# Performance work log

Measured on AMD Instinct MI355X. Metric: run time of the kernel, lower is better.

The kernel has to match this reference:

```python
import jax, jax.numpy as jnp
import numpy as np

N = 100000      # nodes (words + docs)
E = 1600000     # edges
D_IN = 256      # input feature dim
H = 64          # hidden dim
C = 20          # num classes
NDOC = 10000    # doc nodes


def setup_inputs() -> dict:
    key = jax.random.key(0)
    ks = jax.random.split(key, 16)
    inp = {
        "x": jax.random.normal(ks[0], (N, D_IN), dtype=jnp.float32),
        "edge_weight": jax.random.uniform(ks[1], (E,), dtype=jnp.float32),
        "W1": jax.random.normal(ks[2], (D_IN, H), dtype=jnp.float32) * (1.0 / np.sqrt(D_IN)),
        "b1": jnp.zeros((H,), jnp.float32),
        "W2": jax.random.normal(ks[3], (H, H), dtype=jnp.float32) * (1.0 / np.sqrt(H)),
        "b2": jnp.zeros((H,), jnp.float32),
        "W3": jax.random.normal(ks[4], (H, H), dtype=jnp.float32) * (1.0 / np.sqrt(H)),
        "b3": jnp.zeros((H,), jnp.float32),
        "Wp": jax.random.normal(ks[5], (H, H), dtype=jnp.float32) * (1.0 / np.sqrt(H)),
        "bp": jnp.zeros((H,), jnp.float32),
        "Wc": jax.random.normal(ks[6], (H, C), dtype=jnp.float32) * (1.0 / np.sqrt(H)),
        "bc": jnp.zeros((C,), jnp.float32),
        "edge_index": jax.random.randint(ks[7], (2, E), 0, N, dtype=jnp.int32),
        "doc_idx": jnp.sort(jax.random.randint(ks[8], (NDOC,), 0, N, dtype=jnp.int32)),
    }
    return inp


def reference(x, edge_weight, W1, b1, W2, b2, W3, b3, Wp, bp, Wc, bc, edge_index, doc_idx):
    n = x.shape[0]
    src, dst = edge_index[0], edge_index[1]
    loop = jnp.arange(n, dtype=src.dtype)
    rows = jnp.concatenate([src, loop])          # sources (incl. self-loops)
    cols = jnp.concatenate([dst, loop])          # targets
    w = jnp.concatenate([edge_weight, jnp.ones((n,), x.dtype)])
    # symmetric GCN normalization: D^-1/2 (A + I) D^-1/2
    deg = jax.ops.segment_sum(w, cols, num_segments=n)
    deg_safe = jnp.where(deg > 0, deg, 1.0)
    dinv = jnp.where(deg > 0, jax.lax.rsqrt(deg_safe), 0.0)
    norm = dinv[rows] * w * dinv[cols]           # [E+N]

    def conv(h, W, b):
        h = h @ W                                # transform first (PyG GCNConv)
        msg = h[rows] * norm[:, None]            # gather + weight  [E+N, H]
        return jax.ops.segment_sum(msg, cols, num_segments=n) + b

    h = jax.nn.relu(conv(x, W1, b1))             # dropout = identity (eval mode)
    h = jax.nn.relu(conv(h, W2, b2))
    h = jax.nn.relu(conv(h, W3, b3))
    d = h[doc_idx]                               # [NDOC, H]
    d = jax.nn.relu(d @ Wp + bp)
    return d @ Wc + bc                           # [NDOC, C]
```

## Files before the change

kernel.cpp:

```cpp
#include <hip/hip_runtime.h>

#define H 64
#define PAD 48
#define WFIX 262144.0f
#define WFIX_INV (1.0f / 262144.0f)


__global__ __launch_bounds__(256) void k_init(unsigned int* packed, int n) {
    int i = blockIdx.x * 256 + threadIdx.x;
    if (i < n) packed[i] = 0u;
}


__global__ __launch_bounds__(256) void k_fused(const int* __restrict__ src,
                                               const int* __restrict__ dst,
                                               const float* __restrict__ ew,
                                               unsigned int* packed,
                                               int2* __restrict__ csr,
                                               int e_total,
                                               const float* __restrict__ A,
                                               const float* __restrict__ B,
                                               float* __restrict__ out, int M) {
    __shared__ float As[64][68];
    __shared__ float Bs[64][64];
    int tid = threadIdx.x;

    int ebase = blockIdx.x * 1024 + tid;
#pragma unroll
    for (int j = 0; j < 4; ++j) {
        int e = ebase + j * 256;
        if (e < e_total) {
            int d = dst[e];
            float w = ew[e];
            unsigned int enc = (1u << 24) | (unsigned int)(w * WFIX + 0.5f);
            unsigned int old = atomicAdd(&packed[d], enc);
            unsigned int r = old >> 24;
            if (r < PAD) csr[(size_t)d * PAD + r] = make_int2(src[e], __float_as_int(w));
        }
    }

    const int K = 256;
    int brow = blockIdx.x * 64;
    int ct = tid & 15, rt = tid >> 4;
    int c4 = ct * 4, r4 = rt * 4;
    int lrow = tid >> 4;
    int lk4 = (tid & 15) * 4;
    float acc[4][4] = {{0.f}};

    for (int k0 = 0; k0 < K; k0 += 64) {
#pragma unroll
        for (int rr = 0; rr < 64; rr += 16) {
            int row = brow + rr + lrow;
            float4 va = make_float4(0.f, 0.f, 0.f, 0.f);
            if (row < M) va = *(const float4*)&A[(size_t)row * K + k0 + lk4];
            *(float4*)&As[rr + lrow][lk4] = va;
            float4 vb = *(const float4*)&B[(size_t)(k0 + rr + lrow) * 64 + lk4];
            *(float4*)&Bs[rr + lrow][lk4] = vb;
        }
        __syncthreads();
#pragma unroll 16
        for (int kk = 0; kk < 64; ++kk) {
            float4 bv = *(const float4*)&Bs[kk][c4];
#pragma unroll
            for (int i = 0; i < 4; ++i) {
                float av = As[r4 + i][kk];
                acc[i][0] = fmaf(av, bv.x, acc[i][0]);
                acc[i][1] = fmaf(av, bv.y, acc[i][1]);
                acc[i][2] = fmaf(av, bv.z, acc[i][2]);
                acc[i][3] = fmaf(av, bv.w, acc[i][3]);
            }
        }
        __syncthreads();
    }
#pragma unroll
    for (int i = 0; i < 4; ++i) {
        int row = brow + r4 + i;
        if (row < M)
            *(float4*)&out[(size_t)row * H + c4] =
                make_float4(acc[i][0], acc[i][1], acc[i][2], acc[i][3]);
    }
}


__global__ __launch_bounds__(256) void k_scale(const unsigned int* __restrict__ packed,
                                               float* __restrict__ t,
                                               float* __restrict__ dinv, int n) {
    int gid = blockIdx.x * 256 + threadIdx.x;
    if (gid >= n * 16) return;
    int row = gid >> 4, q = gid & 15;
    unsigned int pv = packed[row];
    float di = rsqrtf(1.0f + (float)(pv & 0xFFFFFFu) * WFIX_INV);
    float4 v = *(float4*)&t[(size_t)row * H + q * 4];
    v.x *= di; v.y *= di; v.z *= di; v.w *= di;
    *(float4*)&t[(size_t)row * H + q * 4] = v;
    if (q == 0) dinv[row] = di;
}


__global__ __launch_bounds__(256) void k_agg(const float* __restrict__ t,
                                             float* __restrict__ h,
                                             const int2* __restrict__ csr,
                                             const unsigned int* __restrict__ packed,
                                             const float* __restrict__ dinv,
                                             const float* __restrict__ bias, int n) {
    int wid = (int)((blockIdx.x * 256u + threadIdx.x) >> 6);
    int lane = threadIdx.x & 63;
    if (wid >= n) return;
    float di = dinv[wid];
    int cnt = (int)(packed[wid] >> 24);
    if (cnt > PAD) cnt = PAD;
    const int2* row = &csr[(size_t)wid * PAD];
    float acc = t[(size_t)wid * H + lane];
    int j = 0;
    for (; j + 4 <= cnt; j += 4) {
        int2 e0 = row[j], e1 = row[j + 1], e2 = row[j + 2], e3 = row[j + 3];
        float v0 = t[(size_t)e0.x * H + lane];
        float v1 = t[(size_t)e1.x * H + lane];
        float v2 = t[(size_t)e2.x * H + lane];
        float v3 = t[(size_t)e3.x * H + lane];
        acc = fmaf(v0, __int_as_float(e0.y), acc);
        acc = fmaf(v1, __int_as_float(e1.y), acc);
        acc = fmaf(v2, __int_as_float(e2.y), acc);
        acc = fmaf(v3, __int_as_float(e3.y), acc);
    }
    for (; j < cnt; ++j) {
        int2 e0 = row[j];
        acc = fmaf(t[(size_t)e0.x * H + lane], __int_as_float(e0.y), acc);
    }
    h[(size_t)wid * H + lane] = fmaxf(fmaf(di, acc, bias[lane]), 0.0f);
}


__global__ __launch_bounds__(256) void k_aggdoc(const float* __restrict__ t,
                                                float* __restrict__ dbuf,
                                                const int2* __restrict__ csr,
                                                const unsigned int* __restrict__ packed,
                                                const float* __restrict__ dinv,
                                                const float* __restrict__ bias,
                                                const int* __restrict__ doc, int ndoc) {
    int wid = (int)((blockIdx.x * 256u + threadIdx.x) >> 6);
    int lane = threadIdx.x & 63;
    if (wid >= ndoc) return;
    int d = doc[wid];
    float di = dinv[d];
    int cnt = (int)(packed[d] >> 24);
    if (cnt > PAD) cnt = PAD;
    const int2* row = &csr[(size_t)d * PAD];
    float acc = t[(size_t)d * H + lane];
    int j = 0;
    for (; j + 4 <= cnt; j += 4) {
        int2 e0 = row[j], e1 = row[j + 1], e2 = row[j + 2], e3 = row[j + 3];
        float v0 = t[(size_t)e0.x * H + lane];
        float v1 = t[(size_t)e1.x * H + lane];
        float v2 = t[(size_t)e2.x * H + lane];
        float v3 = t[(size_t)e3.x * H + lane];
        acc = fmaf(v0, __int_as_float(e0.y), acc);
        acc = fmaf(v1, __int_as_float(e1.y), acc);
        acc = fmaf(v2, __int_as_float(e2.y), acc);
        acc = fmaf(v3, __int_as_float(e3.y), acc);
    }
    for (; j < cnt; ++j) {
        int2 e0 = row[j];
        acc = fmaf(t[(size_t)e0.x * H + lane], __int_as_float(e0.y), acc);
    }
    dbuf[(size_t)wid * H + lane] = fmaxf(fmaf(di, acc, bias[lane]), 0.0f);
}


__global__ __launch_bounds__(256) void k_gemm64(const float* __restrict__ A,
                                                const float* __restrict__ B,
                                                float* __restrict__ out,
                                                const float* __restrict__ dinvArr,
                                                int M) {
    __shared__ float As[64][68];
    __shared__ float Bs[64][64];
    int tid = threadIdx.x;
    int brow = blockIdx.x * 64;
    int ct = tid & 15, rt = tid >> 4;
    int c4 = ct * 4, r4 = rt * 4;
    int lrow = tid >> 4;
    int lk4 = (tid & 15) * 4;
    float acc[4][4] = {{0.f}};

#pragma unroll
    for (int rr = 0; rr < 64; rr += 16) {
        int row = brow + rr + lrow;
        float4 va = make_float4(0.f, 0.f, 0.f, 0.f);
        if (row < M) va = *(const float4*)&A[(size_t)row * H + lk4];
        *(float4*)&As[rr + lrow][lk4] = va;
        float4 vb = *(const float4*)&B[(size_t)(rr + lrow) * 64 + lk4];
        *(float4*)&Bs[rr + lrow][lk4] = vb;
    }
    __syncthreads();
#pragma unroll 16
    for (int kk = 0; kk < 64; ++kk) {
        float4 bv = *(const float4*)&Bs[kk][c4];
#pragma unroll
        for (int i = 0; i < 4; ++i) {
            float av = As[r4 + i][kk];
            acc[i][0] = fmaf(av, bv.x, acc[i][0]);
            acc[i][1] = fmaf(av, bv.y, acc[i][1]);
            acc[i][2] = fmaf(av, bv.z, acc[i][2]);
            acc[i][3] = fmaf(av, bv.w, acc[i][3]);
        }
    }
#pragma unroll
    for (int i = 0; i < 4; ++i) {
        int row = brow + r4 + i;
        if (row < M) {
            float sc = dinvArr[row];
            *(float4*)&out[(size_t)row * H + c4] =
                make_float4(acc[i][0] * sc, acc[i][1] * sc, acc[i][2] * sc, acc[i][3] * sc);
        }
    }
}


__global__ __launch_bounds__(256) void k_docgemm(const float* __restrict__ dbuf,
                                                 const float* __restrict__ Wp,
                                                 const float* __restrict__ bp,
                                                 const float* __restrict__ Wc,
                                                 const float* __restrict__ bc,
                                                 float* __restrict__ out,
                                                 int m, int ncls) {
    __shared__ float As[64][68];
    __shared__ float Bs[64][64];
    int tid = threadIdx.x;
    int brow = blockIdx.x * 64;
    int ct = tid & 15, rt = tid >> 4;
    int c4 = ct * 4, r4 = rt * 4;
    int lrow = tid >> 4;
    int lk4 = (tid & 15) * 4;
    float acc[4][4] = {{0.f}};

#pragma unroll
    for (int rr = 0; rr < 64; rr += 16) {
        int row = brow + rr + lrow;
        float4 va = make_float4(0.f, 0.f, 0.f, 0.f);
        if (row < m) va = *(const float4*)&dbuf[(size_t)row * H + lk4];
        *(float4*)&As[rr + lrow][lk4] = va;
        float4 vb = *(const float4*)&Wp[(size_t)(rr + lrow) * 64 + lk4];
        *(float4*)&Bs[rr + lrow][lk4] = vb;
    }
    __syncthreads();
#pragma unroll 16
    for (int kk = 0; kk < 64; ++kk) {
        float4 bv = *(const float4*)&Bs[kk][c4];
#pragma unroll
        for (int i = 0; i < 4; ++i) {
            float av = As[r4 + i][kk];
            acc[i][0] = fmaf(av, bv.x, acc[i][0]);
            acc[i][1] = fmaf(av, bv.y, acc[i][1]);
            acc[i][2] = fmaf(av, bv.z, acc[i][2]);
            acc[i][3] = fmaf(av, bv.w, acc[i][3]);
        }
    }
    __syncthreads();

#pragma unroll
    for (int i = 0; i < 4; ++i) {
        float4 v = make_float4(acc[i][0] + bp[c4],     acc[i][1] + bp[c4 + 1],
                               acc[i][2] + bp[c4 + 2], acc[i][3] + bp[c4 + 3]);
        v.x = fmaxf(v.x, 0.f); v.y = fmaxf(v.y, 0.f);
        v.z = fmaxf(v.z, 0.f); v.w = fmaxf(v.w, 0.f);
        *(float4*)&Bs[r4 + i][c4] = v;
    }
    float* wcs = &As[0][0];
    float* bcs = &As[32][0];
    for (int i = tid; i < H * ncls; i += 256) wcs[i] = Wc[i];
    if (tid < ncls) bcs[tid] = bc[tid];
    __syncthreads();

    for (int o = tid; o < 64 * ncls; o += 256) {
        int r = o / ncls, c = o % ncls;
        int grow = brow + r;
        if (grow >= m) continue;
        float a = bcs[c];
#pragma unroll
        for (int k = 0; k < H; ++k) a = fmaf(Bs[r][k], wcs[k * ncls + c], a);
        out[(size_t)grow * ncls + c] = a;
    }
}


extern "C" void kernel_launch(void* const* d_in, const int* in_sizes, int n_in,
                              void* d_out, int out_size, void* d_ws, size_t ws_size,
                              hipStream_t stream) {
    const float* x  = (const float*)d_in[0];
    const float* ew = (const float*)d_in[1];
    const float* W1 = (const float*)d_in[2];
    const float* b1 = (const float*)d_in[3];
    const float* W2 = (const float*)d_in[4];
    const float* b2 = (const float*)d_in[5];
    const float* W3 = (const float*)d_in[6];
    const float* b3 = (const float*)d_in[7];
    const float* Wp = (const float*)d_in[8];
    const float* bp = (const float*)d_in[9];
    const float* Wc = (const float*)d_in[10];
    const float* bc = (const float*)d_in[11];
    const int*   ei = (const int*)d_in[12];
    const int*  doc = (const int*)d_in[13];
    float* out = (float*)d_out;

    const int DIN  = 256;
    const int n    = in_sizes[0] / DIN;
    const int e    = in_sizes[1];
    const int ndoc = in_sizes[13];
    const int ncls = 20;

    const int* src = ei;
    const int* dst = ei + e;

    char* p = (char*)d_ws;
    auto alloc = [&](size_t bytes) { char* r = p; p += (bytes + 255) & ~(size_t)255; return r; };
    unsigned int* packed = (unsigned int*)alloc((size_t)n * 4);
    float*        dinv   = (float*)alloc((size_t)n * 4);
    int2*         csr    = (int2*)alloc((size_t)n * PAD * 8);
    float*        tbuf   = (float*)alloc((size_t)n * H * 4);
    float*        hbuf   = (float*)alloc((size_t)n * H * 4);
    float*        dbuf   = (float*)alloc((size_t)ndoc * H * 4);

    int nb_n = (n + 255) / 256;
    int nb_g = (n + 63) / 64;
    int nb_s = (n * 16 + 255) / 256;
    int nb_a = (n + 3) / 4;
    int nb_ad = (ndoc + 3) / 4;
    int nb_d  = (ndoc + 63) / 64;

    k_init<<<nb_n, 256, 0, stream>>>(packed, n);
    k_fused<<<nb_g, 256, 0, stream>>>(src, dst, ew, packed, csr, e, x, W1, tbuf, n);
    k_scale<<<nb_s, 256, 0, stream>>>(packed, tbuf, dinv, n);
    k_agg<<<nb_a, 256, 0, stream>>>(tbuf, hbuf, csr, packed, dinv, b1, n);
    k_gemm64<<<nb_g, 256, 0, stream>>>(hbuf, W2, tbuf, dinv, n);
    k_agg<<<nb_a, 256, 0, stream>>>(tbuf, hbuf, csr, packed, dinv, b2, n);
    k_gemm64<<<nb_g, 256, 0, stream>>>(hbuf, W3, tbuf, dinv, n);
    k_aggdoc<<<nb_ad, 256, 0, stream>>>(tbuf, dbuf, csr, packed, dinv, b3, doc, ndoc);
    k_docgemm<<<nb_d, 256, 0, stream>>>(dbuf, Wp, bp, Wc, bc, out, ndoc, ncls);
}
```

Before: 523.8 us.

## Interleave edge atomics with GEMM k-tiles and move source dinv scaling into aggregation

The fused kernel now spreads its CSR-building atomics across the four k-tiles of the first GEMM, so atomic latency overlaps with the shared-memory FMA loop. The k_scale pass over the whole feature matrix becomes a small k_dinv kernel. The source-side normalisation moves from pre-scaled features into the aggregation, which gathers dinv[src] per edge. This removes a full read-write pass over the N×64 buffer and the epilogue scaling in the GEMMs, at the cost of one extra scattered dinv load per edge in every aggregation.

```diff
diff --git a/kernel.cpp b/kernel.cpp
--- a/kernel.cpp
+++ b/kernel.cpp
@@ -25,20 +25,6 @@
     __shared__ float Bs[64][64];
     int tid = threadIdx.x;
 
-    int ebase = blockIdx.x * 1024 + tid;
-#pragma unroll
-    for (int j = 0; j < 4; ++j) {
-        int e = ebase + j * 256;
-        if (e < e_total) {
-            int d = dst[e];
-            float w = ew[e];
-            unsigned int enc = (1u << 24) | (unsigned int)(w * WFIX + 0.5f);
-            unsigned int old = atomicAdd(&packed[d], enc);
-            unsigned int r = old >> 24;
-            if (r < PAD) csr[(size_t)d * PAD + r] = make_int2(src[e], __float_as_int(w));
-        }
-    }
-
     const int K = 256;
     int brow = blockIdx.x * 64;
     int ct = tid & 15, rt = tid >> 4;
@@ -47,7 +33,15 @@
     int lk4 = (tid & 15) * 4;
     float acc[4][4] = {{0.f}};
 
-    for (int k0 = 0; k0 < K; k0 += 64) {
+    int ebase = blockIdx.x * 1024 + tid;
+
+    for (int t4 = 0; t4 < 4; ++t4) {
+        int k0 = t4 * 64;
+        int e = ebase + t4 * 256;
+        bool ok = e < e_total;
+        int ed = 0, es = 0; float w = 0.f;
+        if (ok) { ed = dst[e]; es = src[e]; w = ew[e]; }
+
 #pragma unroll
         for (int rr = 0; rr < 64; rr += 16) {
             int row = brow + rr + lrow;
@@ -58,6 +52,13 @@
             *(float4*)&Bs[rr + lrow][lk4] = vb;
         }
         __syncthreads();
+
+        unsigned int old = 0;
+        if (ok) {
+            unsigned int enc = (1u << 24) | (unsigned int)(w * WFIX + 0.5f);
+            old = atomicAdd(&packed[ed], enc);
+        }
+
 #pragma unroll 16
         for (int kk = 0; kk < 64; ++kk) {
             float4 bv = *(const float4*)&Bs[kk][c4];
@@ -70,8 +71,14 @@
                 acc[i][3] = fmaf(av, bv.w, acc[i][3]);
             }
         }
+
+        if (ok) {
+            unsigned int r = old >> 24;
+            if (r < PAD) csr[(size_t)ed * PAD + r] = make_int2(es, __float_as_int(w));
+        }
         __syncthreads();
     }
+
 #pragma unroll
     for (int i = 0; i < 4; ++i) {
         int row = brow + r4 + i;
@@ -82,18 +89,13 @@
 }
 
 
-__global__ __launch_bounds__(256) void k_scale(const unsigned int* __restrict__ packed,
-                                               float* __restrict__ t,
-                                               float* __restrict__ dinv, int n) {
-    int gid = blockIdx.x * 256 + threadIdx.x;
-    if (gid >= n * 16) return;
-    int row = gid >> 4, q = gid & 15;
-    unsigned int pv = packed[row];
-    float di = rsqrtf(1.0f + (float)(pv & 0xFFFFFFu) * WFIX_INV);
-    float4 v = *(float4*)&t[(size_t)row * H + q * 4];
-    v.x *= di; v.y *= di; v.z *= di; v.w *= di;
-    *(float4*)&t[(size_t)row * H + q * 4] = v;
-    if (q == 0) dinv[row] = di;
+__global__ __launch_bounds__(256) void k_dinv(const unsigned int* __restrict__ packed,
+                                              float* __restrict__ dinv, int n) {
+    int i = blockIdx.x * 256 + threadIdx.x;
+    if (i < n) {
+        unsigned int pv = packed[i];
+        dinv[i] = rsqrtf(1.0f + (float)(pv & 0xFFFFFFu) * WFIX_INV);
+    }
 }
 
 
@@ -110,22 +112,26 @@
     int cnt = (int)(packed[wid] >> 24);
     if (cnt > PAD) cnt = PAD;
     const int2* row = &csr[(size_t)wid * PAD];
-    float acc = t[(size_t)wid * H + lane];
+    float acc = t[(size_t)wid * H + lane] * di;
     int j = 0;
     for (; j + 4 <= cnt; j += 4) {
         int2 e0 = row[j], e1 = row[j + 1], e2 = row[j + 2], e3 = row[j + 3];
+        float m0 = __int_as_float(e0.y) * dinv[e0.x];
+        float m1 = __int_as_float(e1.y) * dinv[e1.x];
+        float m2 = __int_as_float(e2.y) * dinv[e2.x];
+        float m3 = __int_as_float(e3.y) * dinv[e3.x];
         float v0 = t[(size_t)e0.x * H + lane];
         float v1 = t[(size_t)e1.x * H + lane];
         float v2 = t[(size_t)e2.x * H + lane];
         float v3 = t[(size_t)e3.x * H + lane];
-        acc = fmaf(v0, __int_as_float(e0.y), acc);
-        acc = fmaf(v1, __int_as_float(e1.y), acc);
-        acc = fmaf(v2, __int_as_float(e2.y), acc);
-        acc = fmaf(v3, __int_as_float(e3.y), acc);
+        acc = fmaf(v0, m0, acc);
+        acc = fmaf(v1, m1, acc);
+        acc = fmaf(v2, m2, acc);
+        acc = fmaf(v3, m3, acc);
     }
     for (; j < cnt; ++j) {
         int2 e0 = row[j];
-        acc = fmaf(t[(size_t)e0.x * H + lane], __int_as_float(e0.y), acc);
+        acc = fmaf(t[(size_t)e0.x * H + lane], __int_as_float(e0.y) * dinv[e0.x], acc);
     }
     h[(size_t)wid * H + lane] = fmaxf(fmaf(di, acc, bias[lane]), 0.0f);
 }
@@ -146,22 +152,26 @@
     int cnt = (int)(packed[d] >> 24);
     if (cnt > PAD) cnt = PAD;
     const int2* row = &csr[(size_t)d * PAD];
-    float acc = t[(size_t)d * H + lane];
+    float acc = t[(size_t)d * H + lane] * di;
     int j = 0;
     for (; j + 4 <= cnt; j += 4) {
         int2 e0 = row[j], e1 = row[j + 1], e2 = row[j + 2], e3 = row[j + 3];
+        float m0 = __int_as_float(e0.y) * dinv[e0.x];
+        float m1 = __int_as_float(e1.y) * dinv[e1.x];
+        float m2 = __int_as_float(e2.y) * dinv[e2.x];
+        float m3 = __int_as_float(e3.y) * dinv[e3.x];
         float v0 = t[(size_t)e0.x * H + lane];
         float v1 = t[(size_t)e1.x * H + lane];
         float v2 = t[(size_t)e2.x * H + lane];
         float v3 = t[(size_t)e3.x * H + lane];
-        acc = fmaf(v0, __int_as_float(e0.y), acc);
-        acc = fmaf(v1, __int_as_float(e1.y), acc);
-        acc = fmaf(v2, __int_as_float(e2.y), acc);
-        acc = fmaf(v3, __int_as_float(e3.y), acc);
+        acc = fmaf(v0, m0, acc);
+        acc = fmaf(v1, m1, acc);
+        acc = fmaf(v2, m2, acc);
+        acc = fmaf(v3, m3, acc);
     }
     for (; j < cnt; ++j) {
         int2 e0 = row[j];
-        acc = fmaf(t[(size_t)e0.x * H + lane], __int_as_float(e0.y), acc);
+        acc = fmaf(t[(size_t)e0.x * H + lane], __int_as_float(e0.y) * dinv[e0.x], acc);
     }
     dbuf[(size_t)wid * H + lane] = fmaxf(fmaf(di, acc, bias[lane]), 0.0f);
 }
@@ -169,9 +179,7 @@
 
 __global__ __launch_bounds__(256) void k_gemm64(const float* __restrict__ A,
                                                 const float* __restrict__ B,
-                                                float* __restrict__ out,
-                                                const float* __restrict__ dinvArr,
-                                                int M) {
+                                                float* __restrict__ out, int M) {
     __shared__ float As[64][68];
     __shared__ float Bs[64][64];
     int tid = threadIdx.x;
@@ -207,11 +215,9 @@
 #pragma unroll
     for (int i = 0; i < 4; ++i) {
         int row = brow + r4 + i;
-        if (row < M) {
-            float sc = dinvArr[row];
+        if (row < M)
             *(float4*)&out[(size_t)row * H + c4] =
-                make_float4(acc[i][0] * sc, acc[i][1] * sc, acc[i][2] * sc, acc[i][3] * sc);
-        }
+                make_float4(acc[i][0], acc[i][1], acc[i][2], acc[i][3]);
     }
 }
 
@@ -322,18 +328,17 @@
 
     int nb_n = (n + 255) / 256;
     int nb_g = (n + 63) / 64;
-    int nb_s = (n * 16 + 255) / 256;
     int nb_a = (n + 3) / 4;
     int nb_ad = (ndoc + 3) / 4;
     int nb_d  = (ndoc + 63) / 64;
 
     k_init<<<nb_n, 256, 0, stream>>>(packed, n);
     k_fused<<<nb_g, 256, 0, stream>>>(src, dst, ew, packed, csr, e, x, W1, tbuf, n);
-    k_scale<<<nb_s, 256, 0, stream>>>(packed, tbuf, dinv, n);
+    k_dinv<<<nb_n, 256, 0, stream>>>(packed, dinv, n);
     k_agg<<<nb_a, 256, 0, stream>>>(tbuf, hbuf, csr, packed, dinv, b1, n);
-    k_gemm64<<<nb_g, 256, 0, stream>>>(hbuf, W2, tbuf, dinv, n);
+    k_gemm64<<<nb_g, 256, 0, stream>>>(hbuf, W2, tbuf, n);
     k_agg<<<nb_a, 256, 0, stream>>>(tbuf, hbuf, csr, packed, dinv, b2, n);
-    k_gemm64<<<nb_g, 256, 0, stream>>>(hbuf, W3, tbuf, dinv, n);
+    k_gemm64<<<nb_g, 256, 0, stream>>>(hbuf, W3, tbuf, n);
     k_aggdoc<<<nb_ad, 256, 0, stream>>>(tbuf, dbuf, csr, packed, dinv, b3, doc, ndoc);
     k_docgemm<<<nb_d, 256, 0, stream>>>(dbuf, Wp, bp, Wc, bc, out, ndoc, ncls);
 }
```

Result: faster. 487.8 us (-6.9%).
